# Optimization experiments

Hardware: AMD Instinct MI355X
Metric: run time of the kernel (lower is better)

## Reference

```python
import jax, jax.numpy as jnp
import numpy as np

NUM_CODES = 4096
CODE_DIM = 256
COMMITMENT_COST = 0.25
EMA_DECAY = 0.99
EPS = 1e-5


def setup_inputs() -> dict:
    key = jax.random.key(0)
    k1, k2, k3 = jax.random.split(key, 3)
    z = jax.random.normal(k1, (32768, CODE_DIM), dtype=jnp.float32)
    # torch init is uniform(-1/K, 1/K); scale a normal similarly for realism
    weight = jax.random.uniform(k2, (NUM_CODES, CODE_DIM), dtype=jnp.float32,
                                minval=-1.0 / NUM_CODES, maxval=1.0 / NUM_CODES)
    ema_cluster_size = jnp.ones((NUM_CODES,), dtype=jnp.float32)
    ema_w = weight + 0.0  # buffer initialized as a clone of the weights
    del k3
    return {"z": z, "weight": weight, "ema_cluster_size": ema_cluster_size, "ema_w": ema_w}


def reference(z, weight, ema_cluster_size, ema_w):
    # ---- distances: ||z||^2 - 2 z E^T + ||E||^2  -> [N, K] ----
    z2 = jnp.sum(z * z, axis=-1, keepdims=True)              # [N, 1]
    e2 = jnp.sum(weight * weight, axis=-1)                   # [K]
    d = z2 - 2.0 * (z @ weight.T) + e2                       # [N, K]
    indices = jnp.argmin(d, axis=-1)                         # [N] int
    z_q = weight[indices]                                    # [N, D] gather

    # ---- EMA codebook update (training path, buffers are detached) ----
    counts = jax.ops.segment_sum(jnp.ones_like(indices, dtype=z.dtype), indices,
                                 num_segments=NUM_CODES)     # [K]
    dw = jax.ops.segment_sum(z, indices, num_segments=NUM_CODES)  # [K, D]
    new_cs = EMA_DECAY * ema_cluster_size + (1.0 - EMA_DECAY) * counts
    n = jnp.sum(new_cs)
    new_cs = (new_cs + EPS) / (n + NUM_CODES * EPS) * n      # Laplace smoothing
    new_ema_w = EMA_DECAY * ema_w + (1.0 - EMA_DECAY) * dw
    new_weight = new_ema_w / new_cs[:, None]

    # ---- commitment loss + straight-through estimator ----
    vq_loss = COMMITMENT_COST * jnp.mean((z - jax.lax.stop_gradient(z_q)) ** 2)
    z_q_ste = z + jax.lax.stop_gradient(z_q - z)

    return z_q_ste, indices, vq_loss, new_weight, new_cs, new_ema_w
```

## Files before the change

### kernel.cpp

```cpp
#include <hip/hip_runtime.h>
#include <hip/hip_bf16.h>

#define N_ROWS 32768
#define K_CODES 4096
#define D_DIM 256
#define CAP 128
#define MARGIN_T 1e-3f
#define SLOTS 8

#define WS_COUNTS    0
#define WS_LOSSP     16384
#define WS_IDX       147456
#define WS_Z2        278528
#define WS_E2        409600
#define WS_DW        688128

#define DO_ZB        0
#define DO_WB        16777216
#define DO_CAND      18874368
#define DO_CNT8      35651584
#define DO_LMAX      36175872

typedef __attribute__((ext_vector_type(8)))  short bf16x8;
typedef __attribute__((ext_vector_type(16))) float f32x16;
typedef __attribute__((ext_vector_type(8)))  unsigned short us8;

__global__ void k1_norms(const float* __restrict__ z, const float* __restrict__ w,
                         float* __restrict__ z2, float* __restrict__ e2)
{
#pragma clang fp contract(off)
    int gid = blockIdx.x * blockDim.x + threadIdx.x;
    const float* row;
    float* outp;
    if (gid < N_ROWS) { row = z + (size_t)gid * D_DIM; outp = z2 + gid; }
    else if (gid < N_ROWS + K_CODES) { row = w + (size_t)(gid - N_ROWS) * D_DIM; outp = e2 + (gid - N_ROWS); }
    else return;

    float total = 0.0f;
    for (int half = 0; half < 2; half++) {
        const float* x = row + half * 128;
        float r[8];
#pragma unroll
        for (int j = 0; j < 8; j++) { float v = x[j]; r[j] = v * v; }
        for (int i = 8; i < 128; i += 8) {
#pragma unroll
            for (int j = 0; j < 8; j++) { float v = x[i + j]; r[j] += v * v; }
        }
        float s = ((r[0] + r[1]) + (r[2] + r[3])) + ((r[4] + r[5]) + (r[6] + r[7]));
        if (half == 0) total = s; else total = total + s;
    }
    *outp = total;
}

__device__ inline unsigned short f2b(float f) {
    __hip_bfloat16 h = __float2bfloat16(f);
    return *(unsigned short*)&h;
}

__global__ void kconv(const float* __restrict__ z, const float* __restrict__ w,
                      unsigned short* __restrict__ zb, unsigned short* __restrict__ wb)
{
    const int lane  = threadIdx.x & 63;
    const int gwave = blockIdx.x * 4 + (threadIdx.x >> 6);
    const int kk    = gwave & 7;
    const int row   = (gwave >> 3) * 64 + lane;
    const float* src;
    unsigned short* panel;
    int g;
    if (row < N_ROWS) {
        src   = z + (size_t)row * D_DIM;
        panel = zb + ((size_t)((row >> 8) * 8 + kk) << 13);
        g     = (row >> 5) & 7;
    } else {
        int c = row - N_ROWS;
        src   = w + (size_t)c * D_DIM;
        panel = wb + ((size_t)((c >> 8) * 8 + kk) << 13);
        g     = (c >> 5) & 7;
    }
    const int r31 = row & 31;
    const float* s0 = src + kk * 32;
#pragma unroll
    for (int s = 0; s < 2; s++)
#pragma unroll
        for (int h = 0; h < 2; h++) {
            float4 a = *(const float4*)(s0 + s * 16 + h * 8);
            float4 b = *(const float4*)(s0 + s * 16 + h * 8 + 4);
            us8 o;
            o[0] = f2b(a.x); o[1] = f2b(a.y); o[2] = f2b(a.z); o[3] = f2b(a.w);
            o[4] = f2b(b.x); o[5] = f2b(b.y); o[6] = f2b(b.z); o[7] = f2b(b.w);
            *(us8*)(panel + (((g * 2 + s) * 64 + h * 32 + r31) << 3)) = o;
        }
}

__device__ inline void gload16(const void* g, void* l)
{
    __builtin_amdgcn_global_load_lds(
        (const __attribute__((address_space(1))) unsigned int*)g,
        (__attribute__((address_space(3))) unsigned int*)l,
        16, 0, 0);
}

__global__ __launch_bounds__(512, 2) void k2_scan(
    const unsigned short* __restrict__ zb, const unsigned short* __restrict__ wb,
    unsigned char* __restrict__ cnt8, unsigned int* __restrict__ cand2,
    float* __restrict__ lmax)
{
    __shared__ char smem[65536];
    const int tid  = threadIdx.x;
    const int lane = tid & 63;
    const int wid  = tid >> 6;
    const int wm   = wid >> 2;
    const int wn   = wid & 3;
    const int m    = lane & 31;
    const int half = lane >> 5;

    const int r_hw = blockIdx.y * 16 + blockIdx.x;
    const int o    = (r_hw & 7) * 256 + (r_hw >> 3);
    const int cb   = o & 15;
    const int rb   = o >> 4;
    const int rowBase  = rb * 256;
    const int codeBase = cb * 256;

    auto stage = [&](int kk, int buf) {
        char* Ab = smem + buf * 32768;
        char* Bb = Ab + 16384;
        const unsigned short* Ap = wb + ((size_t)(cb * 8 + kk) << 13);
        const unsigned short* Bp = zb + ((size_t)(rb * 8 + kk) << 13);
#pragma unroll
        for (int i = 0; i < 2; i++) {
            gload16(Ap + (size_t)((i * 512 + tid) << 3), Ab + (size_t)(i * 512 + tid) * 16);
            gload16(Bp + (size_t)((i * 512 + tid) << 3), Bb + (size_t)(i * 512 + tid) * 16);
        }
    };

    f32x16 acc[4][2];
    {
        f32x16 zz = {};
#pragma unroll
        for (int ms = 0; ms < 4; ms++)
#pragma unroll
            for (int ns = 0; ns < 2; ns++) acc[ms][ns] = zz;
    }

    stage(0, 0);

    for (int kk = 0; kk < 8; kk++) {
        const int buf = kk & 1;
        __syncthreads();
        if (kk + 1 < 8) stage(kk + 1, buf ^ 1);
        const char* Ab = smem + buf * 32768;
        const char* Bb = Ab + 16384;
#pragma unroll
        for (int s = 0; s < 2; s++) {
            bf16x8 af[4], bfr[2];
#pragma unroll
            for (int ms = 0; ms < 4; ms++)
                af[ms] = *(const bf16x8*)(Ab + (size_t)(((wm * 4 + ms) * 2 + s) * 64 + lane) * 16);
#pragma unroll
            for (int ns = 0; ns < 2; ns++)
                bfr[ns] = *(const bf16x8*)(Bb + (size_t)(((wn * 2 + ns) * 2 + s) * 64 + lane) * 16);
#pragma unroll
            for (int ms = 0; ms < 4; ms++)
#pragma unroll
                for (int ns = 0; ns < 2; ns++)
                    acc[ms][ns] = __builtin_amdgcn_mfma_f32_32x32x16_bf16(
                        af[ms], bfr[ns], acc[ms][ns], 0, 0, 0);
        }
    }

    float tmax[2] = {-1e30f, -1e30f};
#pragma unroll
    for (int ms = 0; ms < 4; ms++)
#pragma unroll
        for (int ns = 0; ns < 2; ns++)
#pragma unroll
            for (int r = 0; r < 16; r++)
                tmax[ns] = fmaxf(tmax[ns], acc[ms][ns][r]);
#pragma unroll
    for (int ns = 0; ns < 2; ns++)
        tmax[ns] = fmaxf(tmax[ns], __shfl_xor(tmax[ns], 32));

    __syncthreads();
    float* rmx  = (float*)smem;
    int*   lcnt = (int*)(smem + 2048);
    if (lane < 32) {
        rmx[wm * 256 + wn * 64 + 0 * 32 + lane] = tmax[0];
        rmx[wm * 256 + wn * 64 + 1 * 32 + lane] = tmax[1];
    }
    if (tid < 256) lcnt[tid] = 0;
    __syncthreads();

    float thr[2];
#pragma unroll
    for (int ns = 0; ns < 2; ns++) {
        const int lr = wn * 64 + ns * 32 + m;
        thr[ns] = fmaxf(rmx[lr], rmx[256 + lr]) - MARGIN_T;
    }

#pragma unroll
    for (int ms = 0; ms < 4; ms++)
#pragma unroll
        for (int ns = 0; ns < 2; ns++)
#pragma unroll
            for (int r = 0; r < 16; r++) {
                float v = acc[ms][ns][r];
                if (v >= thr[ns]) {
                    const int lr = wn * 64 + ns * 32 + m;
                    int slot = atomicAdd(&lcnt[lr], 1);
                    if (slot < SLOTS) {
                        int code = codeBase + wm * 128 + ms * 32
                                 + ((r & 3) + 8 * (r >> 2) + 4 * half);
                        int b = __float_as_int(v);
                        unsigned key = (unsigned)b ^ ((unsigned)(b >> 31) | 0x80000000u);
                        unsigned entry = (key & 0xFFFFF000u) | (unsigned)code;
                        cand2[((size_t)(rowBase + lr) * 16 + cb) * SLOTS + slot] = entry;
                    }
                }
            }

    __syncthreads();
    if (tid < 256) {
        int cf = lcnt[tid];
        cnt8[(size_t)(rowBase + tid) * 16 + cb] =
            (cf > SLOTS) ? (unsigned char)255 : (unsigned char)cf;
        lmax[(size_t)(rowBase + tid) * 16 + cb] = fmaxf(rmx[tid], rmx[256 + tid]);
    }
}

__global__ __launch_bounds__(256) void k_rescore(
    const float* __restrict__ z, const float* __restrict__ w,
    const float* __restrict__ z2, const float* __restrict__ e2,
    const unsigned char* __restrict__ cnt8, const unsigned int* __restrict__ cand2,
    const float* __restrict__ lmax, int* __restrict__ idx_out)
{
#pragma clang fp contract(off)
    const int lane = threadIdx.x & 63;
    const int wv   = threadIdx.x >> 6;
    const int n    = blockIdx.x * 4 + wv;

    __shared__ float4 zst[4][64];
    __shared__ int    surv[4][CAP];

    zst[wv][lane] = ((const float4*)(z + (size_t)n * D_DIM))[lane];

    int   c  = 0;
    float lm = -1e30f;
    if (lane < 16) {
        c  = cnt8[(size_t)n * 16 + lane];
        lm = lmax[(size_t)n * 16 + lane];
    }
    float gm = lm;
#pragma unroll
    for (int off = 32; off > 0; off >>= 1)
        gm = fmaxf(gm, __shfl_xor(gm, off));

    unsigned long long obal =
        __ballot((lane < 16) && (c == 255) && (lm >= gm - MARGIN_T));

    float bd = __builtin_inff(); int bk = K_CODES;
    const float z2v = z2[n];

    {
        const unsigned e0 = cand2[(size_t)n * 128 + lane];
        const unsigned e1 = cand2[(size_t)n * 128 + 64 + lane];
        const int craw0 = __shfl(c, lane >> 3);
        const int craw1 = __shfl(c, 8 + (lane >> 3));
        const int cl0 = (craw0 == 255) ? SLOTS : craw0;
        const int cl1 = (craw1 == 255) ? SLOTS : craw1;
        const float thrF = gm - MARGIN_T - 1e-4f;

        auto keyf = [](unsigned e) -> float {
            unsigned ky = e & 0xFFFFF000u;
            int b = (ky & 0x80000000u) ? (int)(ky ^ 0x80000000u) : (int)~ky;
            return __int_as_float(b);
        };
        const bool keep0 = ((lane & 7) < cl0) && (keyf(e0) >= thrF);
        const bool keep1 = ((lane & 7) < cl1) && (keyf(e1) >= thrF);

        unsigned long long bal0 = __ballot(keep0);
        unsigned long long bal1 = __ballot(keep1);
        const unsigned long long below = (1ull << lane) - 1ull;
        const int n0 = (int)__popcll(bal0);
        if (keep0) surv[wv][(int)__popcll(bal0 & below)] = (int)(e0 & 0xFFFu);
        if (keep1) surv[wv][n0 + (int)__popcll(bal1 & below)] = (int)(e1 & 0xFFFu);
        const int nt = n0 + (int)__popcll(bal1);

        for (int s = lane; s < nt; s += 64) {
            int k = surv[wv][s];
            if ((unsigned)k >= (unsigned)K_CODES) k = 0;
            const float4* wp = (const float4*)(w + (size_t)k * D_DIM);
            float tacc = 0.0f;
#pragma unroll 8
            for (int d4 = 0; d4 < 64; d4++) {
                float4 wvv = wp[d4];
                float4 zv  = zst[wv][d4];
                tacc = __builtin_fmaf(zv.x, wvv.x, tacc);
                tacc = __builtin_fmaf(zv.y, wvv.y, tacc);
                tacc = __builtin_fmaf(zv.z, wvv.z, tacc);
                tacc = __builtin_fmaf(zv.w, wvv.w, tacc);
            }
            float u  = z2v - 2.0f * tacc;
            float dv = u + e2[k];
            if (dv < bd || (dv == bd && k < bk)) { bd = dv; bk = k; }
        }
    }

    while (obal) {
        const int cbq = (int)(__ffsll((long long)obal) - 1);
        obal &= obal - 1ull;
        const int k0 = cbq * 256 + lane;
        const float4* w0 = (const float4*)(w + (size_t)(k0      ) * D_DIM);
        const float4* w1 = (const float4*)(w + (size_t)(k0 +  64) * D_DIM);
        const float4* w2 = (const float4*)(w + (size_t)(k0 + 128) * D_DIM);
        const float4* w3 = (const float4*)(w + (size_t)(k0 + 192) * D_DIM);
        float t0 = 0.0f, t1 = 0.0f, t2 = 0.0f, t3 = 0.0f;
#pragma unroll 8
        for (int d4 = 0; d4 < 64; d4++) {
            float4 zv = zst[wv][d4];
            float4 a0 = w0[d4];
            float4 a1 = w1[d4];
            float4 a2 = w2[d4];
            float4 a3 = w3[d4];
            t0 = __builtin_fmaf(zv.x, a0.x, t0);
            t1 = __builtin_fmaf(zv.x, a1.x, t1);
            t2 = __builtin_fmaf(zv.x, a2.x, t2);
            t3 = __builtin_fmaf(zv.x, a3.x, t3);
            t0 = __builtin_fmaf(zv.y, a0.y, t0);
            t1 = __builtin_fmaf(zv.y, a1.y, t1);
            t2 = __builtin_fmaf(zv.y, a2.y, t2);
            t3 = __builtin_fmaf(zv.y, a3.y, t3);
            t0 = __builtin_fmaf(zv.z, a0.z, t0);
            t1 = __builtin_fmaf(zv.z, a1.z, t1);
            t2 = __builtin_fmaf(zv.z, a2.z, t2);
            t3 = __builtin_fmaf(zv.z, a3.z, t3);
            t0 = __builtin_fmaf(zv.w, a0.w, t0);
            t1 = __builtin_fmaf(zv.w, a1.w, t1);
            t2 = __builtin_fmaf(zv.w, a2.w, t2);
            t3 = __builtin_fmaf(zv.w, a3.w, t3);
        }
        float d0 = (z2v - 2.0f * t0) + e2[k0];
        float d1 = (z2v - 2.0f * t1) + e2[k0 + 64];
        float d2 = (z2v - 2.0f * t2) + e2[k0 + 128];
        float d3 = (z2v - 2.0f * t3) + e2[k0 + 192];
        if (d0 < bd || (d0 == bd && k0       < bk)) { bd = d0; bk = k0; }
        if (d1 < bd || (d1 == bd && k0 +  64 < bk)) { bd = d1; bk = k0 + 64; }
        if (d2 < bd || (d2 == bd && k0 + 128 < bk)) { bd = d2; bk = k0 + 128; }
        if (d3 < bd || (d3 == bd && k0 + 192 < bk)) { bd = d3; bk = k0 + 192; }
    }

#pragma unroll
    for (int off = 1; off < 64; off <<= 1) {
        float od = __shfl_xor(bd, off);
        int   ok = __shfl_xor(bk, off);
        if (od < bd || (od == bd && ok < bk)) { bd = od; bk = ok; }
    }
    if (lane == 0) idx_out[n] = (bk < K_CODES) ? bk : 0;
}

__global__ void k3_scatter(const float* __restrict__ z, const float* __restrict__ w,
                           const int* __restrict__ idx_in,
                           float* __restrict__ counts, float* __restrict__ lossp,
                           float* __restrict__ dw, float* __restrict__ out_zq,
                           float* __restrict__ out_idx)
{
#pragma clang fp contract(off)
    const int n = blockIdx.x;
    const int t = threadIdx.x;
    int idx = idx_in[n];
    if (idx < 0) idx = 0;
    if (idx >= K_CODES) idx = K_CODES - 1;
    if (t == 0) {
        out_idx[n] = (float)idx;
        atomicAdd(&counts[idx], 1.0f);
    }
    float zv = z[(size_t)n * D_DIM + t];
    float wq = w[(size_t)idx * D_DIM + t];
    out_zq[(size_t)n * D_DIM + t] = zv + (wq - zv);
    float df = zv - wq;
    float sq = df * df;
    atomicAdd(&dw[(size_t)idx * D_DIM + t], zv);

    __shared__ float red[256];
    red[t] = sq; __syncthreads();
    for (int s = 128; s > 0; s >>= 1) {
        if (t < s) red[t] += red[t + s];
        __syncthreads();
    }
    if (t == 0) lossp[n] = red[0];
}

__global__ void k4_cs(const float* __restrict__ lossp, const float* __restrict__ counts,
                      const float* __restrict__ cs_in, float* __restrict__ out_loss,
                      float* __restrict__ out_cs)
{
#pragma clang fp contract(off)
    const int t = threadIdx.x;
    __shared__ float red[1024];
    __shared__ float pre[K_CODES];

    float s = 0.0f;
    for (int i = t; i < N_ROWS; i += 1024) s += lossp[i];
    red[t] = s; __syncthreads();
    for (int st = 512; st > 0; st >>= 1) {
        if (t < st) red[t] += red[t + st];
        __syncthreads();
    }
    if (t == 0) out_loss[0] = 0.25f * (red[0] / 8388608.0f);
    __syncthreads();

    const float DEC = 0.99f;
    const float OMD = (float)(1.0 - 0.99);
    float mine[4];
#pragma unroll
    for (int q = 0; q < 4; q++) {
        int k = t + q * 1024;
        float t1 = DEC * cs_in[k];
        float t2 = OMD * counts[k];
        float p = t1 + t2;
        pre[k] = p; mine[q] = p;
    }
    float psum = (mine[0] + mine[1]) + (mine[2] + mine[3]);
    red[t] = psum; __syncthreads();
    for (int st = 512; st > 0; st >>= 1) {
        if (t < st) red[t] += red[t + st];
        __syncthreads();
    }
    float nsum = red[0];
    const float KEPS = (float)(4096.0 * 1e-5);
    float denom = nsum + KEPS;
#pragma unroll
    for (int q = 0; q < 4; q++) {
        int k = t + q * 1024;
        float v = ((pre[k] + 1e-5f) / denom) * nsum;
        out_cs[k] = v;
    }
}

__global__ void k5_emaw(const float* __restrict__ ema_w, const float* __restrict__ dw,
                        const float* __restrict__ newcs, float* __restrict__ out_w,
                        float* __restrict__ out_emaw)
{
#pragma clang fp contract(off)
    const int i = blockIdx.x * 256 + threadIdx.x;
    const int k = i >> 8;
    const float OMD = (float)(1.0 - 0.99);
    float t1 = 0.99f * ema_w[i];
    float t2 = OMD * dw[i];
    float ne = t1 + t2;
    out_emaw[i] = ne;
    out_w[i] = ne / newcs[k];
}

extern "C" void kernel_launch(void* const* d_in, const int* in_sizes, int n_in,
                              void* d_out, int out_size, void* d_ws, size_t ws_size,
                              hipStream_t stream)
{
    const float* z    = (const float*)d_in[0];
    const float* w    = (const float*)d_in[1];
    const float* cs   = (const float*)d_in[2];
    const float* emaw = (const float*)d_in[3];

    float* out      = (float*)d_out;
    float* out_zq   = out;
    float* out_idx  = out + 8388608;
    float* out_loss = out + 8421376;
    float* out_w    = out + 8421377;
    float* out_cs   = out + 9469953;
    float* out_emaw = out + 9474049;

    char* ws = (char*)d_ws;
    float*          counts  = (float*)(ws + WS_COUNTS);
    float*          lossp   = (float*)(ws + WS_LOSSP);
    int*            idx_int = (int*)  (ws + WS_IDX);
    float*          z2      = (float*)(ws + WS_Z2);
    float*          e2      = (float*)(ws + WS_E2);
    float*          dw      = (float*)(ws + WS_DW);

    char* ob = (char*)d_out;
    unsigned short* zb    = (unsigned short*)(ob + DO_ZB);
    unsigned short* wb    = (unsigned short*)(ob + DO_WB);
    unsigned int*   cand2 = (unsigned int*)  (ob + DO_CAND);
    unsigned char*  cnt8  = (unsigned char*) (ob + DO_CNT8);
    float*          lmx   = (float*)         (ob + DO_LMAX);

    hipMemsetAsync(counts, 0, K_CODES * sizeof(float), stream);
    hipMemsetAsync(dw, 0, (size_t)K_CODES * D_DIM * sizeof(float), stream);

    k1_norms<<<(N_ROWS + K_CODES) / 256, 256, 0, stream>>>(z, w, z2, e2);

    kconv<<<1152, 256, 0, stream>>>(z, w, zb, wb);

    dim3 g2(16, 128);
    k2_scan<<<g2, 512, 0, stream>>>(zb, wb, cnt8, cand2, lmx);

    k_rescore<<<N_ROWS / 4, 256, 0, stream>>>(z, w, z2, e2, cnt8, cand2, lmx, idx_int);

    k3_scatter<<<N_ROWS, 256, 0, stream>>>(z, w, idx_int, counts, lossp,
                                           dw, out_zq, out_idx);

    k4_cs<<<1, 1024, 0, stream>>>(lossp, counts, cs, out_loss, out_cs);

    k5_emaw<<<K_CODES, 256, 0, stream>>>(emaw, dw, out_cs, out_w, out_emaw);
}
```

Before: 372.1 us.

## Replace atomic scatter-add of codebook sums with counting-sort gather per code

Instead of having every row atomically add its z vector into dw, the indices are histogrammed, prefix-summed and bucketed into per-code row lists. Each code block then sums its assigned rows directly in the EMA kernel. This removes 8M float atomics and the 4MB dw memset, at the cost of three small extra kernels. It also risks load imbalance when many rows map to a single code, since one block loops serially over them. Summation order now depends on atomic cursor order, which is nondeterministic.

```diff
diff --git a/kernel.cpp b/kernel.cpp
--- a/kernel.cpp
+++ b/kernel.cpp
@@ -13,6 +13,10 @@
 #define WS_IDX       147456
 #define WS_Z2        278528
 #define WS_E2        409600
+#define WS_CCOUNT    425984
+#define WS_STARTS    442368
+#define WS_CURSOR    458752
+#define WS_ROWS      475136
 #define WS_DW        688128
 
 #define DO_ZB        0
@@ -357,10 +361,58 @@
     if (lane == 0) idx_out[n] = (bk < K_CODES) ? bk : 0;
 }
 
+__global__ void k_hist(const int* __restrict__ idx_in, int* __restrict__ ccount)
+{
+    int n = blockIdx.x * 256 + threadIdx.x;
+    int idx = idx_in[n];
+    if (idx < 0) idx = 0;
+    if (idx >= K_CODES) idx = K_CODES - 1;
+    atomicAdd(&ccount[idx], 1);
+}
+
+__global__ void k_prefix(const int* __restrict__ ccount,
+                         int* __restrict__ starts, int* __restrict__ cursor)
+{
+    __shared__ int s[1024];
+    const int t = threadIdx.x;
+    int c0 = ccount[t * 4 + 0];
+    int c1 = ccount[t * 4 + 1];
+    int c2 = ccount[t * 4 + 2];
+    int c3 = ccount[t * 4 + 3];
+    int tsum = ((c0 + c1) + (c2 + c3));
+    s[t] = tsum;
+    __syncthreads();
+    for (int off = 1; off < 1024; off <<= 1) {
+        int v = (t >= off) ? s[t - off] : 0;
+        __syncthreads();
+        s[t] += v;
+        __syncthreads();
+    }
+    int base = s[t] - tsum;
+    starts[t * 4 + 0] = base;
+    starts[t * 4 + 1] = base + c0;
+    starts[t * 4 + 2] = base + c0 + c1;
+    starts[t * 4 + 3] = base + c0 + c1 + c2;
+    cursor[t * 4 + 0] = base;
+    cursor[t * 4 + 1] = base + c0;
+    cursor[t * 4 + 2] = base + c0 + c1;
+    cursor[t * 4 + 3] = base + c0 + c1 + c2;
+}
+
+__global__ void k_fill(const int* __restrict__ idx_in, int* __restrict__ cursor,
+                       int* __restrict__ rows)
+{
+    int n = blockIdx.x * 256 + threadIdx.x;
+    int idx = idx_in[n];
+    if (idx < 0) idx = 0;
+    if (idx >= K_CODES) idx = K_CODES - 1;
+    int pos = atomicAdd(&cursor[idx], 1);
+    rows[pos] = n;
+}
+
 __global__ void k3_scatter(const float* __restrict__ z, const float* __restrict__ w,
                            const int* __restrict__ idx_in,
-                           float* __restrict__ counts, float* __restrict__ lossp,
-                           float* __restrict__ dw, float* __restrict__ out_zq,
+                           float* __restrict__ lossp, float* __restrict__ out_zq,
                            float* __restrict__ out_idx)
 {
 #pragma clang fp contract(off)
@@ -369,16 +421,13 @@
     int idx = idx_in[n];
     if (idx < 0) idx = 0;
     if (idx >= K_CODES) idx = K_CODES - 1;
-    if (t == 0) {
-        out_idx[n] = (float)idx;
-        atomicAdd(&counts[idx], 1.0f);
-    }
+    if (t == 0) out_idx[n] = (float)idx;
+
     float zv = z[(size_t)n * D_DIM + t];
     float wq = w[(size_t)idx * D_DIM + t];
     out_zq[(size_t)n * D_DIM + t] = zv + (wq - zv);
     float df = zv - wq;
     float sq = df * df;
-    atomicAdd(&dw[(size_t)idx * D_DIM + t], zv);
 
     __shared__ float red[256];
     red[t] = sq; __syncthreads();
@@ -389,7 +438,7 @@
     if (t == 0) lossp[n] = red[0];
 }
 
-__global__ void k4_cs(const float* __restrict__ lossp, const float* __restrict__ counts,
+__global__ void k4_cs(const float* __restrict__ lossp, const int* __restrict__ ccount,
                       const float* __restrict__ cs_in, float* __restrict__ out_loss,
                       float* __restrict__ out_cs)
 {
@@ -415,7 +464,7 @@
     for (int q = 0; q < 4; q++) {
         int k = t + q * 1024;
         float t1 = DEC * cs_in[k];
-        float t2 = OMD * counts[k];
+        float t2 = OMD * (float)ccount[k];
         float p = t1 + t2;
         pre[k] = p; mine[q] = p;
     }
@@ -436,19 +485,29 @@
     }
 }
 
-__global__ void k5_emaw(const float* __restrict__ ema_w, const float* __restrict__ dw,
-                        const float* __restrict__ newcs, float* __restrict__ out_w,
-                        float* __restrict__ out_emaw)
+__global__ void k5_emaw(const float* __restrict__ z, const float* __restrict__ ema_w,
+                        const int* __restrict__ starts, const int* __restrict__ ccount,
+                        const int* __restrict__ rows, const float* __restrict__ newcs,
+                        float* __restrict__ out_w, float* __restrict__ out_emaw)
 {
 #pragma clang fp contract(off)
-    const int i = blockIdx.x * 256 + threadIdx.x;
-    const int k = i >> 8;
+    const int k = blockIdx.x;
+    const int t = threadIdx.x;
+    const int s = starts[k];
+    const int e = s + ccount[k];
+
+    float acc = 0.0f;
+    for (int r = s; r < e; r++) {
+        int row = rows[r];
+        acc += z[(size_t)row * D_DIM + t];
+    }
+
     const float OMD = (float)(1.0 - 0.99);
-    float t1 = 0.99f * ema_w[i];
-    float t2 = OMD * dw[i];
+    float t1 = 0.99f * ema_w[(size_t)k * D_DIM + t];
+    float t2 = OMD * acc;
     float ne = t1 + t2;
-    out_emaw[i] = ne;
-    out_w[i] = ne / newcs[k];
+    out_emaw[(size_t)k * D_DIM + t] = ne;
+    out_w[(size_t)k * D_DIM + t] = ne / newcs[k];
 }
 
 extern "C" void kernel_launch(void* const* d_in, const int* in_sizes, int n_in,
@@ -469,12 +528,14 @@
     float* out_emaw = out + 9474049;
 
     char* ws = (char*)d_ws;
-    float*          counts  = (float*)(ws + WS_COUNTS);
     float*          lossp   = (float*)(ws + WS_LOSSP);
     int*            idx_int = (int*)  (ws + WS_IDX);
     float*          z2      = (float*)(ws + WS_Z2);
     float*          e2      = (float*)(ws + WS_E2);
-    float*          dw      = (float*)(ws + WS_DW);
+    int*            ccount  = (int*)  (ws + WS_CCOUNT);
+    int*            starts  = (int*)  (ws + WS_STARTS);
+    int*            cursor  = (int*)  (ws + WS_CURSOR);
+    int*            rowsb   = (int*)  (ws + WS_ROWS);
 
     char* ob = (char*)d_out;
     unsigned short* zb    = (unsigned short*)(ob + DO_ZB);
@@ -483,8 +544,7 @@
     unsigned char*  cnt8  = (unsigned char*) (ob + DO_CNT8);
     float*          lmx   = (float*)         (ob + DO_LMAX);
 
-    hipMemsetAsync(counts, 0, K_CODES * sizeof(float), stream);
-    hipMemsetAsync(dw, 0, (size_t)K_CODES * D_DIM * sizeof(float), stream);
+    hipMemsetAsync(ccount, 0, K_CODES * sizeof(int), stream);
 
     k1_norms<<<(N_ROWS + K_CODES) / 256, 256, 0, stream>>>(z, w, z2, e2);
 
@@ -495,10 +555,14 @@
 
     k_rescore<<<N_ROWS / 4, 256, 0, stream>>>(z, w, z2, e2, cnt8, cand2, lmx, idx_int);
 
-    k3_scatter<<<N_ROWS, 256, 0, stream>>>(z, w, idx_int, counts, lossp,
-                                           dw, out_zq, out_idx);
-
-    k4_cs<<<1, 1024, 0, stream>>>(lossp, counts, cs, out_loss, out_cs);
-
-    k5_emaw<<<K_CODES, 256, 0, stream>>>(emaw, dw, out_cs, out_w, out_emaw);
-}
+    k_hist<<<N_ROWS / 256, 256, 0, stream>>>(idx_int, ccount);
+    k_prefix<<<1, 1024, 0, stream>>>(ccount, starts, cursor);
+    k_fill<<<N_ROWS / 256, 256, 0, stream>>>(idx_int, cursor, rowsb);
+
+    k3_scatter<<<N_ROWS, 256, 0, stream>>>(z, w, idx_int, lossp, out_zq, out_idx);
+
+    k4_cs<<<1, 1024, 0, stream>>>(lossp, ccount, cs, out_loss, out_cs);
+
+    k5_emaw<<<K_CODES, 256, 0, stream>>>(z, emaw, starts, ccount, rowsb,
+                                         out_cs, out_w, out_emaw);
+}
```

After: 381.4 us. 2.5% more time.
